# Optimization experiments

Hardware: AMD Instinct MI355X
Metric: run time of the kernel (lower is better)

Reference implementation:

```python
import jax, jax.numpy as jnp
import numpy as np

# dims
B, T, V, E, H, N, WD, R = 32, 256, 10000, 256, 512, 128, 64, 4
IFACE = R*WD + R + WD + 1 + WD + WD + R + 1 + 1 + 3*R  # concatenated interface vector size
EPS = 1e-6


def setup_inputs() -> dict:
    key = jax.random.key(0)
    ks = jax.random.split(key, 8)
    s = 0.05
    return {
        "tokens": jax.random.randint(ks[0], (B, T), 0, V),
        "emb": jax.random.normal(ks[1], (V, E), jnp.float32) * s,
        "w_ih": jax.random.normal(ks[2], (4*H, E + R*WD), jnp.float32) * s,
        "w_hh": jax.random.normal(ks[3], (4*H, H), jnp.float32) * s,
        "b_lstm": jnp.zeros((4*H,), jnp.float32),
        "W_iface": jax.random.normal(ks[4], (H, IFACE), jnp.float32) * s,
        "b_iface": jnp.zeros((IFACE,), jnp.float32),
        "W_out": jax.random.normal(ks[5], (H + R*WD, V), jnp.float32) * s,
        "b_out": jnp.zeros((V,), jnp.float32),
        "pass_through_memory": 1,
        "reset_experience": 1,
    }


def _cosine(M, k):
    # M: [B,N,W], k: [B,K,W] -> [B,K,N]
    dot = jnp.einsum('bnw,bkw->bkn', M, k)
    Mn = jnp.linalg.norm(M, axis=-1)   # [B,N]
    kn = jnp.linalg.norm(k, axis=-1)   # [B,K]
    return dot / (kn[:, :, None] * Mn[:, None, :] + EPS)


def _dnc_forward(tokens, emb, w_ih, w_hh, b_lstm, W_iface, b_iface, W_out, b_out):
    x = jnp.tanh(emb[tokens])          # [B,T,E] embedding + tanh
    f32 = x.dtype
    eye = jnp.eye(N, dtype=f32)
    carry0 = (
        jnp.zeros((B, H), f32),        # h
        jnp.zeros((B, H), f32),        # c
        jnp.zeros((B, N, WD), f32),    # memory M
        jnp.zeros((B, N, N), f32),     # link matrix L
        jnp.zeros((B, N), f32),        # precedence p
        jnp.zeros((B, N), f32),        # usage u
        jnp.zeros((B, R, N), f32),     # read weights wr
        jnp.zeros((B, N), f32),        # write weights ww
        jnp.zeros((B, R, WD), f32),    # read vectors rv
    )

    def step(carry, x_t):
        h, c, M, L, p, u, wr, ww, rv = carry
        # --- controller LSTM: input = [x_t ; previous read vectors] ---
        inp = jnp.concatenate([x_t, rv.reshape(B, R*WD)], axis=-1)
        gates = inp @ w_ih.T + h @ w_hh.T + b_lstm
        gi, gf, gg, go = jnp.split(gates, 4, axis=-1)
        c = jax.nn.sigmoid(gf)*c + jax.nn.sigmoid(gi)*jnp.tanh(gg)
        h = jax.nn.sigmoid(go)*jnp.tanh(c)
        # --- interface vector (equivalent to independent linears, concatenated) ---
        xi = h @ W_iface + b_iface
        o = 0
        rk = xi[:, o:o+R*WD].reshape(B, R, WD); o += R*WD   # read keys
        rb = 1.0 + jax.nn.softplus(xi[:, o:o+R]); o += R    # read strengths (oneplus)
        wk = xi[:, o:o+WD][:, None, :]; o += WD             # write key [B,1,W]
        wb = 1.0 + jax.nn.softplus(xi[:, o:o+1]); o += 1    # write strength
        er = jax.nn.sigmoid(xi[:, o:o+WD]); o += WD         # erase vector
        wv = xi[:, o:o+WD]; o += WD                         # write vector
        fg = jax.nn.sigmoid(xi[:, o:o+R]); o += R           # free gates
        ga = jax.nn.sigmoid(xi[:, o:o+1]); o += 1           # allocation gate
        gw = jax.nn.sigmoid(xi[:, o:o+1]); o += 1           # write gate
        pi = jax.nn.softmax(xi[:, o:o+3*R].reshape(B, R, 3), axis=-1)  # read modes
        # --- usage / retention ---
        psi = jnp.prod(1.0 - fg[:, :, None]*wr, axis=1)     # [B,N]
        u = (u + ww - u*ww) * psi
        # --- allocation weighting via usage sort ---
        phi = jnp.argsort(u, axis=-1)                       # ascending usage
        u_s = jnp.take_along_axis(u, phi, axis=-1)
        cp = jnp.cumprod(u_s, axis=-1)
        cp_ex = jnp.concatenate([jnp.ones((B, 1), f32), cp[:, :-1]], axis=-1)
        a_s = (1.0 - u_s) * cp_ex
        a = jnp.take_along_axis(a_s, jnp.argsort(phi, axis=-1), axis=-1)
        # --- write weighting (content + allocation) ---
        cw = jax.nn.softmax(wb * _cosine(M, wk)[:, 0, :], axis=-1)  # [B,N]
        ww = gw * (ga*a + (1.0 - ga)*cw)
        # --- memory erase + write (outer products) ---
        M = M * (1.0 - ww[:, :, None]*er[:, None, :]) + ww[:, :, None]*wv[:, None, :]
        # --- temporal link matrix and precedence ---
        L = (1.0 - ww[:, :, None] - ww[:, None, :]) * L + ww[:, :, None]*p[:, None, :]
        L = L * (1.0 - eye)
        p = (1.0 - ww.sum(-1, keepdims=True))*p + ww
        # --- read weighting: backward / content / forward modes ---
        fwdw = jnp.einsum('bnm,brm->brn', L, wr)
        bwdw = jnp.einsum('bmn,brm->brn', L, wr)
        cr = jax.nn.softmax(rb[:, :, None] * _cosine(M, rk), axis=-1)  # [B,R,N]
        wr = pi[..., 0:1]*bwdw + pi[..., 1:2]*cr + pi[..., 2:3]*fwdw
        rv = jnp.einsum('brn,bnw->brw', wr, M)
        out = jnp.concatenate([h, rv.reshape(B, R*WD)], axis=-1) @ W_out + b_out
        return (h, c, M, L, p, u, wr, ww, rv), out

    _, ys = jax.lax.scan(step, carry0, jnp.swapaxes(x, 0, 1))
    return jnp.swapaxes(ys, 0, 1)  # logits [B,T,V]


def reference(tokens, emb, w_ih, w_hh, b_lstm, W_iface, b_iface, W_out, b_out, pass_through_memory, reset_experience):
    # reset_experience=True path: fresh memory state; pass_through_memory=True: full DNC memory.
    return _dnc_forward(tokens, emb, w_ih, w_hh, b_lstm, W_iface, b_iface, W_out, b_out)
```

## Files before the change

kernel.cpp:

```cpp
#include <hip/hip_runtime.h>
#include <math.h>
#include <stdint.h>

#define TB 256
#define NB 32
#define EV 10000
#define ED 256
#define HD 512
#define NM 128
#define WDIM 64
#define RH 4
#define NIF 471
#define CEPS 1e-6f

__device__ __forceinline__ float sigm(float x) { return 1.0f / (1.0f + expf(-x)); }
__device__ __forceinline__ float sofp(float x) { return fmaxf(x, 0.0f) + log1pf(expf(-fabsf(x))); }

__device__ __forceinline__ float red128_max(float v, int tid, float* red2) {
#pragma unroll
  for (int m = 32; m > 0; m >>= 1) v = fmaxf(v, __shfl_xor(v, m));
  if (tid == 0) red2[0] = v;
  if (tid == 64) red2[1] = v;
  __syncthreads();
  float r = fmaxf(red2[0], red2[1]);
  __syncthreads();
  return r;
}
__device__ __forceinline__ float red128_sum(float v, int tid, float* red2) {
#pragma unroll
  for (int m = 32; m > 0; m >>= 1) v += __shfl_xor(v, m);
  if (tid == 0) red2[0] = v;
  if (tid == 64) red2[1] = v;
  __syncthreads();
  float r = red2[0] + red2[1];
  __syncthreads();
  return r;
}

__global__ __launch_bounds__(256) void k_embed(const int* __restrict__ tok,
                                               const float* __restrict__ emb,
                                               float* __restrict__ x) {
  int gid = blockIdx.x * 256 + threadIdx.x;
  int bt = gid >> 8, k = gid & 255;
  int t = tok[bt];
  x[gid] = tanhf(emb[(size_t)t * ED + k]);
}

__global__ __launch_bounds__(256) void k_gates(
    const float* __restrict__ xall, const float* __restrict__ rv,
    const float* __restrict__ h0, float* __restrict__ c,
    const float* __restrict__ wih, const float* __restrict__ whh,
    const float* __restrict__ blstm, float* __restrict__ hrv, int step) {
  __shared__ float U[NB][257];
  __shared__ float G[8][NB];
  const int tid = threadIdx.x;
  const int b = tid & 31, jj = tid >> 5;
  const int ul = jj >> 2, g = jj & 3;
  const int u0 = blockIdx.x * 2;
  const int j = (u0 + ul) + (g << 9);
  float a0 = blstm[j], a1 = 0.f, a2 = 0.f, a3 = 0.f;
  const float* wbase = wih + (size_t)j * 512;
  const float* wbase2 = whh + (size_t)j * 512;
  for (int tile = 0; tile < 4; ++tile) {
#pragma unroll
    for (int i = 0; i < 8; ++i) {
      int f = tid + (i << 8);
      int bb = f >> 6, k = (f & 63) << 2;
      const float* src;
      if (tile == 0)
        src = xall + (((size_t)bb * TB + step) << 8) + k;
      else if (tile == 1)
        src = rv + (bb << 8) + k;
      else {
        const float* hp = step ? (hrv + ((size_t)bb * TB + step - 1) * 768)
                               : (h0 + (bb << 9));
        src = hp + ((tile - 2) << 8) + k;
      }
      float4 v = *reinterpret_cast<const float4*>(src);
      U[bb][k] = v.x; U[bb][k + 1] = v.y; U[bb][k + 2] = v.z; U[bb][k + 3] = v.w;
    }
    __syncthreads();
    const float4* wp = reinterpret_cast<const float4*>(
        (tile < 2 ? wbase : wbase2) + ((tile & 1) << 8));
#pragma unroll 4
    for (int k4 = 0; k4 < 64; ++k4) {
      float4 w4 = wp[k4];
      int k = k4 << 2;
      a0 = fmaf(U[b][k], w4.x, a0);
      a1 = fmaf(U[b][k + 1], w4.y, a1);
      a2 = fmaf(U[b][k + 2], w4.z, a2);
      a3 = fmaf(U[b][k + 3], w4.w, a3);
    }
    __syncthreads();
  }
  G[jj][b] = (a0 + a1) + (a2 + a3);
  __syncthreads();
  if (tid < 64) {
    int u2 = tid >> 5, bb = tid & 31;
    int u = u0 + u2;
    float gi = G[u2 * 4 + 0][bb], gf = G[u2 * 4 + 1][bb];
    float gg = G[u2 * 4 + 2][bb], go = G[u2 * 4 + 3][bb];
    float cold = c[(bb << 9) + u];
    float cn = sigm(gf) * cold + sigm(gi) * tanhf(gg);
    float hn = sigm(go) * tanhf(cn);
    c[(bb << 9) + u] = cn;
    hrv[((size_t)bb * TB + step) * 768 + u] = hn;
  }
}

__global__ __launch_bounds__(1024) void k_mem(
    float* __restrict__ hrv, const float* __restrict__ wif,
    const float* __restrict__ bif, float* __restrict__ M_g,
    float* __restrict__ L_g, float* __restrict__ p_g, float* __restrict__ u_g,
    float* __restrict__ wr_g, float* __restrict__ ww_g,
    float* __restrict__ rv_g, int step) {
  __shared__ float h_s[512];
  __shared__ float xi_s[472];
  __shared__ float xip_s[512][2];
  __shared__ float M_s[NM][65];
  __shared__ float wro_s[4][NM];
  __shared__ float fwd_s[4][NM];
  __shared__ float bwd_s[4][NM];
  __shared__ float crsd_s[4][NM];
  __shared__ float wrn_s[4][NM];
  __shared__ float un_s[NM];
  __shared__ float wwn_s[NM];
  __shared__ float po_s[NM];
  __shared__ float nrmp_s[NM][8];
  __shared__ float nrm_s[NM];
  __shared__ float er_s[WDIM];
  __shared__ float wv_s[WDIM];
  __shared__ float rvp_s[256][5];
  __shared__ float rb_s[4], fg_s[4], rkn_s[4];
  __shared__ float pi_s[12];
  __shared__ float red2[2];
  __shared__ float redw[8];
  __shared__ float hm_s[4], hs_s[4];
  __shared__ float sc_s[4];

  const int tid = threadIdx.x;
  const int b = blockIdx.x;
  const size_t row = (size_t)b * TB + step;
  float* hp = hrv + row * 768;
  float* Mg = M_g + (size_t)b * (NM * WDIM);
  float* Lg = L_g + (size_t)b * (NM * NM);

  if (tid < 512) h_s[tid] = hp[tid];
  for (int f = tid; f < 2048; f += 1024) {
    float4 v = reinterpret_cast<const float4*>(Mg)[f];
    int n = f >> 4, w = (f & 15) << 2;
    M_s[n][w] = v.x; M_s[n][w + 1] = v.y; M_s[n][w + 2] = v.z; M_s[n][w + 3] = v.w;
  }
  if (tid < 512) wro_s[tid >> 7][tid & 127] = wr_g[b * 512 + tid];
  float uo = 0.f, wwo = 0.f;
  if (tid < 128) {
    uo = u_g[b * 128 + tid];
    wwo = ww_g[b * 128 + tid];
    po_s[tid] = p_g[b * 128 + tid];
  }
  __syncthreads();

  {
    int half = tid >> 9, c = tid & 511;
    if (c < NIF) {
      const float* wp = wif + (size_t)(half * 256) * NIF + c;
      const float* hh = h_s + half * 256;
      float a0 = 0.f, a1 = 0.f, a2 = 0.f, a3 = 0.f;
      for (int k = 0; k < 256; k += 4) {
        a0 = fmaf(hh[k + 0], wp[(size_t)(k + 0) * NIF], a0);
        a1 = fmaf(hh[k + 1], wp[(size_t)(k + 1) * NIF], a1);
        a2 = fmaf(hh[k + 2], wp[(size_t)(k + 2) * NIF], a2);
        a3 = fmaf(hh[k + 3], wp[(size_t)(k + 3) * NIF], a3);
      }
      xip_s[c][half] = (a0 + a1) + (a2 + a3);
    }
  }
  __syncthreads();
  if (tid < NIF) xi_s[tid] = bif[tid] + xip_s[tid][0] + xip_s[tid][1];
  __syncthreads();

  if (tid < 64) {
    er_s[tid] = sigm(xi_s[325 + tid]);
    wv_s[tid] = xi_s[389 + tid];
  } else if (tid < 68) {
    rb_s[tid - 64] = 1.0f + sofp(xi_s[256 + (tid - 64)]);
  } else if (tid < 72) {
    fg_s[tid - 68] = sigm(xi_s[453 + (tid - 68)]);
  } else if (tid < 76) {
    int r = tid - 72;
    float nq = 0.f;
    for (int w = 0; w < 64; ++w) { float v = xi_s[r * 64 + w]; nq = fmaf(v, v, nq); }
    rkn_s[r] = sqrtf(nq);
  } else if (tid < 80) {
    int r = tid - 76;
    float e0 = xi_s[459 + 3 * r], e1 = xi_s[460 + 3 * r], e2 = xi_s[461 + 3 * r];
    float mx = fmaxf(e0, fmaxf(e1, e2));
    float p0 = expf(e0 - mx), p1 = expf(e1 - mx), p2 = expf(e2 - mx);
    float s = p0 + p1 + p2;
    pi_s[3 * r] = p0 / s; pi_s[3 * r + 1] = p1 / s; pi_s[3 * r + 2] = p2 / s;
  } else if (tid == 80) {
    sc_s[0] = 1.0f + sofp(xi_s[324]);
  } else if (tid == 81) {
    sc_s[1] = sigm(xi_s[457]);
  } else if (tid == 82) {
    sc_s[2] = sigm(xi_s[458]);
  } else if (tid == 83) {
    float nq = 0.f;
    for (int w = 0; w < 64; ++w) { float v = xi_s[260 + w]; nq = fmaf(v, v, nq); }
    sc_s[3] = sqrtf(nq);
  }
  __syncthreads();

  float score = -1e30f;
  if (tid < 128) {
    int n = tid;
    float psi = 1.0f;
#pragma unroll
    for (int r = 0; r < 4; ++r) psi *= (1.0f - fg_s[r] * wro_s[r][n]);
    float un = (uo + wwo - uo * wwo) * psi;
    un_s[n] = un;
    u_g[b * 128 + n] = un;
    float d0 = 0.f, d1 = 0.f, q0 = 0.f, q1 = 0.f;
#pragma unroll 4
    for (int w = 0; w < 64; w += 2) {
      float m0 = M_s[n][w], m1 = M_s[n][w + 1];
      d0 = fmaf(m0, xi_s[260 + w], d0); q0 = fmaf(m0, m0, q0);
      d1 = fmaf(m1, xi_s[260 + w + 1], d1); q1 = fmaf(m1, m1, q1);
    }
    score = sc_s[0] * (d0 + d1) / (sc_s[3] * sqrtf(q0 + q1) + CEPS);
  }
  __syncthreads();

  float aval = 0.f;
  if (tid < 128) {
    int n = tid;
    float un = un_s[n];
    float p0 = 1.0f, p1 = 1.0f;
#pragma unroll 4
    for (int m = 0; m < 128; m += 2) {
      float u0 = un_s[m], u1 = un_s[m + 1];
      p0 *= ((u0 < un) || (u0 == un && m < n)) ? u0 : 1.0f;
      p1 *= ((u1 < un) || (u1 == un && (m + 1) < n)) ? u1 : 1.0f;
    }
    aval = (1.0f - un) * p0 * p1;
  }
  float gmax = red128_max(score, tid, red2);
  float ev = (tid < 128) ? expf(score - gmax) : 0.f;
  float gsum = red128_sum(ev, tid, red2);
  float wwv = 0.f;
  if (tid < 128) {
    float cw = ev / gsum;
    wwv = sc_s[2] * (sc_s[1] * aval + (1.0f - sc_s[1]) * cw);
    wwn_s[tid] = wwv;
    ww_g[b * 128 + tid] = wwv;
  }
  float sumww = red128_sum(wwv, tid, red2);

  {
    int n = tid >> 3, w0 = (tid & 7) << 3;
    float wn = wwn_s[n];
    float nq = 0.f;
    float mv_[8];
#pragma unroll
    for (int j = 0; j < 8; ++j) {
      int w = w0 + j;
      float mv = M_s[n][w];
      mv = mv * (1.0f - wn * er_s[w]) + wn * wv_s[w];
      M_s[n][w] = mv;
      mv_[j] = mv;
      nq = fmaf(mv, mv, nq);
    }
    nrmp_s[n][tid & 7] = nq;
    float4* mg4 = reinterpret_cast<float4*>(Mg + (n << 6) + w0);
    mg4[0] = make_float4(mv_[0], mv_[1], mv_[2], mv_[3]);
    mg4[1] = make_float4(mv_[4], mv_[5], mv_[6], mv_[7]);
  }
  for (int e = tid; e < NM * NM; e += 1024) {
    int n = e >> 7, m = e & 127;
    float lv = Lg[e];
    float nv = (n == m) ? 0.f
                        : (1.0f - wwn_s[n] - wwn_s[m]) * lv + wwn_s[n] * po_s[m];
    Lg[e] = nv;
  }
  if (tid < 128) p_g[b * 128 + tid] = (1.0f - sumww) * po_s[tid] + wwn_s[tid];
  __syncthreads();

  {
    int type = tid >> 9, r = (tid >> 7) & 3, n = tid & 127;
    const float* wrr = wro_s[r];
    float a0 = 0.f, a1 = 0.f, a2 = 0.f, a3 = 0.f;
    if (type == 0) {
      const float* Lr = Lg + (n << 7);
#pragma unroll 4
      for (int m = 0; m < 128; m += 4) {
        float4 l4 = *reinterpret_cast<const float4*>(Lr + m);
        a0 = fmaf(l4.x, wrr[m + 0], a0);
        a1 = fmaf(l4.y, wrr[m + 1], a1);
        a2 = fmaf(l4.z, wrr[m + 2], a2);
        a3 = fmaf(l4.w, wrr[m + 3], a3);
      }
      fwd_s[r][n] = (a0 + a1) + (a2 + a3);
    } else {
      const float* Lc = Lg + n;
#pragma unroll 4
      for (int m = 0; m < 128; m += 4) {
        a0 = fmaf(Lc[(m + 0) << 7], wrr[m + 0], a0);
        a1 = fmaf(Lc[(m + 1) << 7], wrr[m + 1], a1);
        a2 = fmaf(Lc[(m + 2) << 7], wrr[m + 2], a2);
        a3 = fmaf(Lc[(m + 3) << 7], wrr[m + 3], a3);
      }
      bwd_s[r][n] = (a0 + a1) + (a2 + a3);
    }
  }
  if (tid < 128) {
    float s = 0.f;
#pragma unroll
    for (int j = 0; j < 8; ++j) s += nrmp_s[tid][j];
    nrm_s[tid] = sqrtf(s);
  }
  if (tid < 512) {
    int r = tid >> 7, n = tid & 127;
    const float* xk = xi_s + r * 64;
    float d0 = 0.f, d1 = 0.f, d2 = 0.f, d3 = 0.f;
#pragma unroll 4
    for (int w = 0; w < 64; w += 4) {
      d0 = fmaf(M_s[n][w + 0], xk[w + 0], d0);
      d1 = fmaf(M_s[n][w + 1], xk[w + 1], d1);
      d2 = fmaf(M_s[n][w + 2], xk[w + 2], d2);
      d3 = fmaf(M_s[n][w + 3], xk[w + 3], d3);
    }
    crsd_s[r][n] = (d0 + d1) + (d2 + d3);
  }
  __syncthreads();

  {
    int r = (tid >> 7) & 3, n = tid & 127;
    float v = -1e30f;
    if (tid < 512) v = rb_s[r] * crsd_s[r][n] / (rkn_s[r] * nrm_s[n] + CEPS);
    float mx = v;
#pragma unroll
    for (int m = 32; m > 0; m >>= 1) mx = fmaxf(mx, __shfl_xor(mx, m));
    if ((tid & 63) == 0 && tid < 512) redw[tid >> 6] = mx;
    __syncthreads();
    if (tid < 4) hm_s[tid] = fmaxf(redw[2 * tid], redw[2 * tid + 1]);
    __syncthreads();
    float e = 0.f;
    if (tid < 512) e = expf(v - hm_s[r]);
    float sm = e;
#pragma unroll
    for (int m = 32; m > 0; m >>= 1) sm += __shfl_xor(sm, m);
    if ((tid & 63) == 0 && tid < 512) redw[tid >> 6] = sm;
    __syncthreads();
    if (tid < 4) hs_s[tid] = redw[2 * tid] + redw[2 * tid + 1];
    __syncthreads();
    if (tid < 512) {
      float crn = e / hs_s[r];
      float w = pi_s[3 * r] * bwd_s[r][n] + pi_s[3 * r + 1] * crn +
                pi_s[3 * r + 2] * fwd_s[r][n];
      wrn_s[r][n] = w;
      wr_g[b * 512 + r * 128 + n] = w;
    }
  }
  __syncthreads();

  {
    int out = tid & 255, q = tid >> 8;
    int r = out >> 6, w = out & 63;
    const float* wrr = wrn_s[r];
    int n0 = q << 5;
    float a0 = 0.f, a1 = 0.f;
#pragma unroll 4
    for (int n = n0; n < n0 + 32; n += 2) {
      a0 = fmaf(wrr[n], M_s[n][w], a0);
      a1 = fmaf(wrr[n + 1], M_s[n + 1][w], a1);
    }
    rvp_s[out][q] = a0 + a1;
  }
  __syncthreads();
  if (tid < 256) {
    float acc = rvp_s[tid][0] + rvp_s[tid][1] + rvp_s[tid][2] + rvp_s[tid][3];
    rv_g[b * 256 + tid] = acc;
    hp[512 + tid] = acc;
  }
}

__global__ __launch_bounds__(256) void k_out(const float* __restrict__ A,
                                             const float* __restrict__ W,
                                             const float* __restrict__ bias,
                                             float* __restrict__ C) {
  __shared__ float As[8][128];
  __shared__ float Bs[8][128];
  const int tid = threadIdx.x;
  const int tx = tid & 15, ty = tid >> 4;
  const int m0 = blockIdx.x << 7;
  const int n0 = blockIdx.y << 7;
  float acc[8][8];
#pragma unroll
  for (int i = 0; i < 8; ++i)
#pragma unroll
    for (int j = 0; j < 8; ++j) acc[i][j] = 0.f;
  const int arow = tid >> 1, akk = (tid & 1) << 2;
  const int bk = tid >> 5, bn = (tid & 31) << 2;
  for (int k0 = 0; k0 < 768; k0 += 8) {
    float4 av = *reinterpret_cast<const float4*>(A + (size_t)(m0 + arow) * 768 + k0 + akk);
    float4 bv = make_float4(0.f, 0.f, 0.f, 0.f);
    if (n0 + bn < EV)
      bv = *reinterpret_cast<const float4*>(W + (size_t)(k0 + bk) * EV + n0 + bn);
    __syncthreads();
    As[akk + 0][arow] = av.x; As[akk + 1][arow] = av.y;
    As[akk + 2][arow] = av.z; As[akk + 3][arow] = av.w;
    *reinterpret_cast<float4*>(&Bs[bk][bn]) = bv;
    __syncthreads();
#pragma unroll
    for (int k = 0; k < 8; ++k) {
      float a_[8], b_[8];
#pragma unroll
      for (int i = 0; i < 8; ++i) a_[i] = As[k][ty + (i << 4)];
#pragma unroll
      for (int j = 0; j < 8; ++j) b_[j] = Bs[k][tx + (j << 4)];
#pragma unroll
      for (int i = 0; i < 8; ++i)
#pragma unroll
        for (int j = 0; j < 8; ++j) acc[i][j] = fmaf(a_[i], b_[j], acc[i][j]);
    }
  }
#pragma unroll
  for (int i = 0; i < 8; ++i) {
    int row = m0 + ty + (i << 4);
#pragma unroll
    for (int j = 0; j < 8; ++j) {
      int col = n0 + tx + (j << 4);
      if (col < EV) C[(size_t)row * EV + col] = acc[i][j] + bias[col];
    }
  }
}

extern "C" void kernel_launch(void* const* d_in, const int* in_sizes, int n_in,
                              void* d_out, int out_size, void* d_ws,
                              size_t ws_size, hipStream_t stream) {
  const int* tokens = (const int*)d_in[0];
  const float* emb = (const float*)d_in[1];
  const float* wih = (const float*)d_in[2];
  const float* whh = (const float*)d_in[3];
  const float* blstm = (const float*)d_in[4];
  const float* wif = (const float*)d_in[5];
  const float* bif = (const float*)d_in[6];
  const float* wout = (const float*)d_in[7];
  const float* bout = (const float*)d_in[8];
  float* out = (float*)d_out;

  float* ws = (float*)d_ws;
  float* xall = ws;
  float* hrv = xall + 2097152;
  float* h0 = hrv + 6291456;
  float* cS = h0 + 16384;
  float* MS = cS + 16384;
  float* LS = MS + 262144;
  float* pS = LS + 524288;
  float* uS = pS + 4096;
  float* wrS = uS + 4096;
  float* wwS = wrS + 16384;
  float* rvS = wwS + 4096;

  hipMemsetAsync(h0, 0, (size_t)856064 * sizeof(float), stream);
  k_embed<<<8192, 256, 0, stream>>>(tokens, emb, xall);
  for (int t = 0; t < TB; ++t) {
    k_gates<<<256, 256, 0, stream>>>(xall, rvS, h0, cS, wih, whh, blstm, hrv, t);
    k_mem<<<32, 1024, 0, stream>>>(hrv, wif, bif, MS, LS, pS, uS, wrS, wwS, rvS, t);
  }
  dim3 g(64, 79);
  k_out<<<g, 256, 0, stream>>>(hrv, wout, bout, out);
}
```

Baseline: 16.99 ms.

## Split interface matmul into wide kernel, stage link matrix in LDS, split-K gates

Moves the h·W_iface projection out of the 32-block memory kernel into a separate 236-block kernel that reads a pre-transposed copy of W_iface, so this matvec is spread across many CUs instead of 32. The memory kernel now keeps the link matrix in swizzled dynamic shared memory and computes forward and backward link reads from LDS, sharing each L element across all four read heads. The gates kernel is widened to 1024 threads with a 4-way split over K. The cost is an extra kernel launch per timestep, a one-time transpose, and larger shared memory use that limits blocks per CU.

```diff
diff --git a/kernel.cpp b/kernel.cpp
--- a/kernel.cpp
+++ b/kernel.cpp
@@ -11,6 +11,7 @@
 #define WDIM 64
 #define RH 4
 #define NIF 471
+#define NIFP 480
 #define CEPS 1e-6f
 
 __device__ __forceinline__ float sigm(float x) { return 1.0f / (1.0f + expf(-x)); }
@@ -46,25 +47,32 @@
   x[gid] = tanhf(emb[(size_t)t * ED + k]);
 }
 
-__global__ __launch_bounds__(256) void k_gates(
+__global__ __launch_bounds__(256) void k_wift(const float* __restrict__ wif,
+                                              float* __restrict__ wifT) {
+  int gid = blockIdx.x * 256 + threadIdx.x;
+  int k = gid / NIF, c = gid - k * NIF;
+  wifT[(size_t)c * 512 + k] = wif[gid];
+}
+
+__global__ __launch_bounds__(1024) void k_gates(
     const float* __restrict__ xall, const float* __restrict__ rv,
     const float* __restrict__ h0, float* __restrict__ c,
     const float* __restrict__ wih, const float* __restrict__ whh,
     const float* __restrict__ blstm, float* __restrict__ hrv, int step) {
   __shared__ float U[NB][257];
-  __shared__ float G[8][NB];
+  __shared__ float Gp[4][8][33];
   const int tid = threadIdx.x;
-  const int b = tid & 31, jj = tid >> 5;
+  const int b = tid & 31, jj = (tid >> 5) & 7, kq = tid >> 8;
   const int ul = jj >> 2, g = jj & 3;
   const int u0 = blockIdx.x * 2;
   const int j = (u0 + ul) + (g << 9);
-  float a0 = blstm[j], a1 = 0.f, a2 = 0.f, a3 = 0.f;
+  float a0 = 0.f, a1 = 0.f, a2 = 0.f, a3 = 0.f;
   const float* wbase = wih + (size_t)j * 512;
   const float* wbase2 = whh + (size_t)j * 512;
   for (int tile = 0; tile < 4; ++tile) {
 #pragma unroll
-    for (int i = 0; i < 8; ++i) {
-      int f = tid + (i << 8);
+    for (int i = 0; i < 2; ++i) {
+      int f = tid + (i << 10);
       int bb = f >> 6, k = (f & 63) << 2;
       const float* src;
       if (tile == 0)
@@ -81,11 +89,12 @@
     }
     __syncthreads();
     const float4* wp = reinterpret_cast<const float4*>(
-        (tile < 2 ? wbase : wbase2) + ((tile & 1) << 8));
-#pragma unroll 4
-    for (int k4 = 0; k4 < 64; ++k4) {
+        (tile < 2 ? wbase : wbase2) + ((tile & 1) << 8) + (kq << 6));
+    const int kb = kq << 6;
+#pragma unroll 4
+    for (int k4 = 0; k4 < 16; ++k4) {
       float4 w4 = wp[k4];
-      int k = k4 << 2;
+      int k = kb + (k4 << 2);
       a0 = fmaf(U[b][k], w4.x, a0);
       a1 = fmaf(U[b][k + 1], w4.y, a1);
       a2 = fmaf(U[b][k + 2], w4.z, a2);
@@ -93,36 +102,82 @@
     }
     __syncthreads();
   }
-  G[jj][b] = (a0 + a1) + (a2 + a3);
+  Gp[kq][jj][b] = (a0 + a1) + (a2 + a3);
   __syncthreads();
   if (tid < 64) {
     int u2 = tid >> 5, bb = tid & 31;
     int u = u0 + u2;
-    float gi = G[u2 * 4 + 0][bb], gf = G[u2 * 4 + 1][bb];
-    float gg = G[u2 * 4 + 2][bb], go = G[u2 * 4 + 3][bb];
+    float gv[4];
+#pragma unroll
+    for (int g2 = 0; g2 < 4; ++g2) {
+      int jj2 = u2 * 4 + g2;
+      gv[g2] = blstm[u + (g2 << 9)] + Gp[0][jj2][bb] + Gp[1][jj2][bb] +
+               Gp[2][jj2][bb] + Gp[3][jj2][bb];
+    }
     float cold = c[(bb << 9) + u];
-    float cn = sigm(gf) * cold + sigm(gi) * tanhf(gg);
-    float hn = sigm(go) * tanhf(cn);
+    float cn = sigm(gv[1]) * cold + sigm(gv[0]) * tanhf(gv[2]);
+    float hn = sigm(gv[3]) * tanhf(cn);
     c[(bb << 9) + u] = cn;
     hrv[((size_t)bb * TB + step) * 768 + u] = hn;
   }
 }
 
+__global__ __launch_bounds__(256) void k_iface(
+    const float* __restrict__ hrv, const float* __restrict__ wifT,
+    const float* __restrict__ bif, float* __restrict__ xi_g, int step) {
+  __shared__ float xp[4][2][33];
+  const int tid = threadIdx.x;
+  const int b = tid & 31, cl = (tid >> 5) & 1, kq = tid >> 6;
+  const int c = blockIdx.x * 2 + cl;
+  float a0 = 0.f, a1 = 0.f, a2 = 0.f, a3 = 0.f;
+  if (c < NIF) {
+    const float4* hp4 = reinterpret_cast<const float4*>(
+        hrv + ((size_t)b * TB + step) * 768 + (kq << 7));
+    const float4* wp4 =
+        reinterpret_cast<const float4*>(wifT + (size_t)c * 512 + (kq << 7));
+#pragma unroll 4
+    for (int k4 = 0; k4 < 32; ++k4) {
+      float4 h4 = hp4[k4];
+      float4 w4 = wp4[k4];
+      a0 = fmaf(h4.x, w4.x, a0);
+      a1 = fmaf(h4.y, w4.y, a1);
+      a2 = fmaf(h4.z, w4.z, a2);
+      a3 = fmaf(h4.w, w4.w, a3);
+    }
+  }
+  xp[kq][cl][b] = (a0 + a1) + (a2 + a3);
+  __syncthreads();
+  if (tid < 64) {
+    int bb = tid & 31, cl2 = tid >> 5;
+    int c2 = blockIdx.x * 2 + cl2;
+    if (c2 < NIF) {
+      float v = bif[c2] + xp[0][cl2][bb] + xp[1][cl2][bb] + xp[2][cl2][bb] +
+                xp[3][cl2][bb];
+      xi_g[bb * NIFP + c2] = v;
+    }
+  }
+}
+
+#define MS(n, w) Ms[(n) * 65 + (w)]
+#define LIDX(n, m) (((n) << 7) + ((m) ^ (((n)&7) << 2)))
+
 __global__ __launch_bounds__(1024) void k_mem(
-    float* __restrict__ hrv, const float* __restrict__ wif,
-    const float* __restrict__ bif, float* __restrict__ M_g,
-    float* __restrict__ L_g, float* __restrict__ p_g, float* __restrict__ u_g,
-    float* __restrict__ wr_g, float* __restrict__ ww_g,
-    float* __restrict__ rv_g, int step) {
-  __shared__ float h_s[512];
+    float* __restrict__ hrv, const float* __restrict__ xi_g,
+    float* __restrict__ M_g, float* __restrict__ L_g, float* __restrict__ p_g,
+    float* __restrict__ u_g, float* __restrict__ wr_g,
+    float* __restrict__ ww_g, float* __restrict__ rv_g, int step) {
+  extern __shared__ float dyn[];
+  float* Ls = dyn;
+  float* Ms = dyn + 16384;
+
   __shared__ float xi_s[472];
-  __shared__ float xip_s[512][2];
-  __shared__ float M_s[NM][65];
   __shared__ float wro_s[4][NM];
   __shared__ float fwd_s[4][NM];
   __shared__ float bwd_s[4][NM];
   __shared__ float crsd_s[4][NM];
   __shared__ float wrn_s[4][NM];
+  __shared__ float fwdp[4][4][NM];
+  __shared__ float bwdp[4][4][NM];
   __shared__ float un_s[NM];
   __shared__ float wwn_s[NM];
   __shared__ float po_s[NM];
@@ -145,11 +200,15 @@
   float* Mg = M_g + (size_t)b * (NM * WDIM);
   float* Lg = L_g + (size_t)b * (NM * NM);
 
-  if (tid < 512) h_s[tid] = hp[tid];
   for (int f = tid; f < 2048; f += 1024) {
     float4 v = reinterpret_cast<const float4*>(Mg)[f];
     int n = f >> 4, w = (f & 15) << 2;
-    M_s[n][w] = v.x; M_s[n][w + 1] = v.y; M_s[n][w + 2] = v.z; M_s[n][w + 3] = v.w;
+    MS(n, w) = v.x; MS(n, w + 1) = v.y; MS(n, w + 2) = v.z; MS(n, w + 3) = v.w;
+  }
+  for (int f = tid; f < 4096; f += 1024) {
+    float4 v = reinterpret_cast<const float4*>(Lg)[f];
+    int n = f >> 5, m = (f & 31) << 2;
+    *reinterpret_cast<float4*>(&Ls[LIDX(n, m)]) = v;
   }
   if (tid < 512) wro_s[tid >> 7][tid & 127] = wr_g[b * 512 + tid];
   float uo = 0.f, wwo = 0.f;
@@ -158,25 +217,7 @@
     wwo = ww_g[b * 128 + tid];
     po_s[tid] = p_g[b * 128 + tid];
   }
-  __syncthreads();
-
-  {
-    int half = tid >> 9, c = tid & 511;
-    if (c < NIF) {
-      const float* wp = wif + (size_t)(half * 256) * NIF + c;
-      const float* hh = h_s + half * 256;
-      float a0 = 0.f, a1 = 0.f, a2 = 0.f, a3 = 0.f;
-      for (int k = 0; k < 256; k += 4) {
-        a0 = fmaf(hh[k + 0], wp[(size_t)(k + 0) * NIF], a0);
-        a1 = fmaf(hh[k + 1], wp[(size_t)(k + 1) * NIF], a1);
-        a2 = fmaf(hh[k + 2], wp[(size_t)(k + 2) * NIF], a2);
-        a3 = fmaf(hh[k + 3], wp[(size_t)(k + 3) * NIF], a3);
-      }
-      xip_s[c][half] = (a0 + a1) + (a2 + a3);
-    }
-  }
-  __syncthreads();
-  if (tid < NIF) xi_s[tid] = bif[tid] + xip_s[tid][0] + xip_s[tid][1];
+  if (tid < NIF) xi_s[tid] = xi_g[b * NIFP + tid];
   __syncthreads();
 
   if (tid < 64) {
@@ -223,7 +264,7 @@
     float d0 = 0.f, d1 = 0.f, q0 = 0.f, q1 = 0.f;
 #pragma unroll 4
     for (int w = 0; w < 64; w += 2) {
-      float m0 = M_s[n][w], m1 = M_s[n][w + 1];
+      float m0 = MS(n, w), m1 = MS(n, w + 1);
       d0 = fmaf(m0, xi_s[260 + w], d0); q0 = fmaf(m0, m0, q0);
       d1 = fmaf(m1, xi_s[260 + w + 1], d1); q1 = fmaf(m1, m1, q1);
     }
@@ -262,12 +303,12 @@
     float nq = 0.f;
     float mv_[8];
 #pragma unroll
-    for (int j = 0; j < 8; ++j) {
-      int w = w0 + j;
-      float mv = M_s[n][w];
+    for (int jx = 0; jx < 8; ++jx) {
+      int w = w0 + jx;
+      float mv = MS(n, w);
       mv = mv * (1.0f - wn * er_s[w]) + wn * wv_s[w];
-      M_s[n][w] = mv;
-      mv_[j] = mv;
+      MS(n, w) = mv;
+      mv_[jx] = mv;
       nq = fmaf(mv, mv, nq);
     }
     nrmp_s[n][tid & 7] = nq;
@@ -275,61 +316,76 @@
     mg4[0] = make_float4(mv_[0], mv_[1], mv_[2], mv_[3]);
     mg4[1] = make_float4(mv_[4], mv_[5], mv_[6], mv_[7]);
   }
-  for (int e = tid; e < NM * NM; e += 1024) {
-    int n = e >> 7, m = e & 127;
-    float lv = Lg[e];
-    float nv = (n == m) ? 0.f
-                        : (1.0f - wwn_s[n] - wwn_s[m]) * lv + wwn_s[n] * po_s[m];
-    Lg[e] = nv;
+  for (int f = tid; f < 4096; f += 1024) {
+    int n = f >> 5, m = (f & 31) << 2;
+    float4* lp = reinterpret_cast<float4*>(&Ls[LIDX(n, m)]);
+    float4 lv = *lp;
+    float wn = wwn_s[n];
+    float4 nv;
+    nv.x = (n == m + 0) ? 0.f : (1.f - wn - wwn_s[m + 0]) * lv.x + wn * po_s[m + 0];
+    nv.y = (n == m + 1) ? 0.f : (1.f - wn - wwn_s[m + 1]) * lv.y + wn * po_s[m + 1];
+    nv.z = (n == m + 2) ? 0.f : (1.f - wn - wwn_s[m + 2]) * lv.z + wn * po_s[m + 2];
+    nv.w = (n == m + 3) ? 0.f : (1.f - wn - wwn_s[m + 3]) * lv.w + wn * po_s[m + 3];
+    *lp = nv;
+    reinterpret_cast<float4*>(Lg)[f] = nv;
   }
   if (tid < 128) p_g[b * 128 + tid] = (1.0f - sumww) * po_s[tid] + wwn_s[tid];
   __syncthreads();
 
-  {
-    int type = tid >> 9, r = (tid >> 7) & 3, n = tid & 127;
-    const float* wrr = wro_s[r];
-    float a0 = 0.f, a1 = 0.f, a2 = 0.f, a3 = 0.f;
-    if (type == 0) {
-      const float* Lr = Lg + (n << 7);
-#pragma unroll 4
-      for (int m = 0; m < 128; m += 4) {
-        float4 l4 = *reinterpret_cast<const float4*>(Lr + m);
-        a0 = fmaf(l4.x, wrr[m + 0], a0);
-        a1 = fmaf(l4.y, wrr[m + 1], a1);
-        a2 = fmaf(l4.z, wrr[m + 2], a2);
-        a3 = fmaf(l4.w, wrr[m + 3], a3);
-      }
-      fwd_s[r][n] = (a0 + a1) + (a2 + a3);
-    } else {
-      const float* Lc = Lg + n;
-#pragma unroll 4
-      for (int m = 0; m < 128; m += 4) {
-        a0 = fmaf(Lc[(m + 0) << 7], wrr[m + 0], a0);
-        a1 = fmaf(Lc[(m + 1) << 7], wrr[m + 1], a1);
-        a2 = fmaf(Lc[(m + 2) << 7], wrr[m + 2], a2);
-        a3 = fmaf(Lc[(m + 3) << 7], wrr[m + 3], a3);
-      }
-      bwd_s[r][n] = (a0 + a1) + (a2 + a3);
-    }
-  }
-  if (tid < 128) {
-    float s = 0.f;
-#pragma unroll
-    for (int j = 0; j < 8; ++j) s += nrmp_s[tid][j];
-    nrm_s[tid] = sqrtf(s);
-  }
   if (tid < 512) {
-    int r = tid >> 7, n = tid & 127;
+    int q = tid >> 7, n = tid & 127;
+    int m0 = q << 5;
+    float f0 = 0, f1 = 0, f2 = 0, f3 = 0, g0 = 0, g1 = 0, g2 = 0, g3 = 0;
+#pragma unroll
+    for (int m = m0; m < m0 + 32; m += 4) {
+      float4 l4 = *reinterpret_cast<const float4*>(&Ls[LIDX(n, m)]);
+      f0 = fmaf(l4.x, wro_s[0][m], f0);     f0 = fmaf(l4.y, wro_s[0][m + 1], f0);
+      f0 = fmaf(l4.z, wro_s[0][m + 2], f0); f0 = fmaf(l4.w, wro_s[0][m + 3], f0);
+      f1 = fmaf(l4.x, wro_s[1][m], f1);     f1 = fmaf(l4.y, wro_s[1][m + 1], f1);
+      f1 = fmaf(l4.z, wro_s[1][m + 2], f1); f1 = fmaf(l4.w, wro_s[1][m + 3], f1);
+      f2 = fmaf(l4.x, wro_s[2][m], f2);     f2 = fmaf(l4.y, wro_s[2][m + 1], f2);
+      f2 = fmaf(l4.z, wro_s[2][m + 2], f2); f2 = fmaf(l4.w, wro_s[2][m + 3], f2);
+      f3 = fmaf(l4.x, wro_s[3][m], f3);     f3 = fmaf(l4.y, wro_s[3][m + 1], f3);
+      f3 = fmaf(l4.z, wro_s[3][m + 2], f3); f3 = fmaf(l4.w, wro_s[3][m + 3], f3);
+    }
+#pragma unroll 4
+    for (int m = m0; m < m0 + 32; ++m) {
+      float lv = Ls[LIDX(m, n)];
+      g0 = fmaf(lv, wro_s[0][m], g0);
+      g1 = fmaf(lv, wro_s[1][m], g1);
+      g2 = fmaf(lv, wro_s[2][m], g2);
+      g3 = fmaf(lv, wro_s[3][m], g3);
+    }
+    fwdp[q][0][n] = f0; fwdp[q][1][n] = f1; fwdp[q][2][n] = f2; fwdp[q][3][n] = f3;
+    bwdp[q][0][n] = g0; bwdp[q][1][n] = g1; bwdp[q][2][n] = g2; bwdp[q][3][n] = g3;
+  } else {
+    int s = tid - 512;
+    int r = s >> 7, n = s & 127;
     const float* xk = xi_s + r * 64;
     float d0 = 0.f, d1 = 0.f, d2 = 0.f, d3 = 0.f;
 #pragma unroll 4
     for (int w = 0; w < 64; w += 4) {
-      d0 = fmaf(M_s[n][w + 0], xk[w + 0], d0);
-      d1 = fmaf(M_s[n][w + 1], xk[w + 1], d1);
-      d2 = fmaf(M_s[n][w + 2], xk[w + 2], d2);
-      d3 = fmaf(M_s[n][w + 3], xk[w + 3], d3);
+      d0 = fmaf(MS(n, w + 0), xk[w + 0], d0);
+      d1 = fmaf(MS(n, w + 1), xk[w + 1], d1);
+      d2 = fmaf(MS(n, w + 2), xk[w + 2], d2);
+      d3 = fmaf(MS(n, w + 3), xk[w + 3], d3);
     }
     crsd_s[r][n] = (d0 + d1) + (d2 + d3);
+  }
+  __syncthreads();
+  {
+    int r = (tid >> 7) & 3, n = tid & 127;
+    if (tid < 512) {
+      fwd_s[r][n] = fwdp[0][r][n] + fwdp[1][r][n] + fwdp[2][r][n] + fwdp[3][r][n];
+      if (tid < 128) {
+        float s = 0.f;
+#pragma unroll
+        for (int jx = 0; jx < 8; ++jx) s += nrmp_s[tid][jx];
+        nrm_s[tid] = sqrtf(s);
+      }
+    } else {
+      bwd_s[r][n] = bwdp[0][r][n] + bwdp[1][r][n] + bwdp[2][r][n] + bwdp[3][r][n];
+    }
   }
   __syncthreads();
 
@@ -371,8 +427,8 @@
     float a0 = 0.f, a1 = 0.f;
 #pragma unroll 4
     for (int n = n0; n < n0 + 32; n += 2) {
-      a0 = fmaf(wrr[n], M_s[n][w], a0);
-      a1 = fmaf(wrr[n + 1], M_s[n + 1][w], a1);
+      a0 = fmaf(wrr[n], MS(n, w), a0);
+      a1 = fmaf(wrr[n + 1], MS(n + 1, w), a1);
     }
     rvp_s[out][q] = a0 + a1;
   }
@@ -454,19 +510,31 @@
   float* hrv = xall + 2097152;
   float* h0 = hrv + 6291456;
   float* cS = h0 + 16384;
-  float* MS = cS + 16384;
-  float* LS = MS + 262144;
-  float* pS = LS + 524288;
+  float* MS_ = cS + 16384;
+  float* LS_ = MS_ + 262144;
+  float* pS = LS_ + 524288;
   float* uS = pS + 4096;
   float* wrS = uS + 4096;
   float* wwS = wrS + 16384;
   float* rvS = wwS + 4096;
+  float* xiS = h0 + 856064;
+  float* wifT = xiS + 15360;
+
+  static bool attr_set = false;
+  if (!attr_set) {
+    hipFuncSetAttribute(reinterpret_cast<const void*>(k_mem),
+                        hipFuncAttributeMaxDynamicSharedMemorySize, 98816);
+    attr_set = true;
+  }
 
   hipMemsetAsync(h0, 0, (size_t)856064 * sizeof(float), stream);
+  k_wift<<<942, 256, 0, stream>>>(wif, wifT);
   k_embed<<<8192, 256, 0, stream>>>(tokens, emb, xall);
   for (int t = 0; t < TB; ++t) {
-    k_gates<<<256, 256, 0, stream>>>(xall, rvS, h0, cS, wih, whh, blstm, hrv, t);
-    k_mem<<<32, 1024, 0, stream>>>(hrv, wif, bif, MS, LS, pS, uS, wrS, wwS, rvS, t);
+    k_gates<<<256, 1024, 0, stream>>>(xall, rvS, h0, cS, wih, whh, blstm, hrv, t);
+    k_iface<<<236, 256, 0, stream>>>(hrv, wifT, bif, xiS, t);
+    k_mem<<<32, 1024, 98816, stream>>>(hrv, xiS, MS_, LS_, pS, uS, wrS, wwS,
+                                       rvS, t);
   }
   dim3 g(64, 79);
   k_out<<<g, 256, 0, stream>>>(hrv, wout, bout, out);
```

New measurement: 15.53 ms. 1.09x faster.
